# Kernel tuning notes

Measured on AMD Instinct MI355X. Metric: run time of the kernel, lower is better.

## Reference

```python
import jax, jax.numpy as jnp
import numpy as np

EMBED_DIM = 2048
NUM_HEADS = 16
NUM_HEADS_KV = 16
HEAD_DIM = EMBED_DIM // NUM_HEADS  # 128
ROT_DIM = HEAD_DIM // 2            # rotary_emb_dim = 64 (partial rotary)
ROPE_BASE = 10000.0
SEQLEN = 2048


def _rope_cos_sin(seqlen):
    # inv_freq over rotary dim (fp32 positions, as pos_idx_in_fp32=True)
    inv_freq = 1.0 / (ROPE_BASE ** (jnp.arange(0, ROT_DIM, 2, dtype=jnp.float32) / ROT_DIM))
    t = jnp.arange(seqlen, dtype=jnp.float32)
    freqs = jnp.outer(t, inv_freq)                 # (S, ROT_DIM//2)
    return jnp.cos(freqs), jnp.sin(freqs)


def _apply_rotary(x, cos, sin):
    # x: (B, S, H, D); non-interleaved (GPT-NeoX) rotary on first ROT_DIM dims
    rd = cos.shape[-1] * 2
    x_rot, x_pass = x[..., :rd], x[..., rd:]
    x1, x2 = x_rot[..., : rd // 2], x_rot[..., rd // 2 :]
    c = cos[None, :, None, :]
    s = sin[None, :, None, :]
    o1 = x1 * c - x2 * s
    o2 = x1 * s + x2 * c
    return jnp.concatenate([o1, o2, x_pass], axis=-1)


def setup_inputs() -> dict:
    key = jax.random.key(0)
    ks = jax.random.split(key, 5)
    scale_in = 1.0 / np.sqrt(EMBED_DIM)
    return {
        "x_q": jax.random.normal(ks[0], (SEQLEN, EMBED_DIM), dtype=jnp.float32),
        "Wqkv_w": jax.random.normal(ks[1], (HEAD_DIM * (NUM_HEADS + 2 * NUM_HEADS_KV), EMBED_DIM), dtype=jnp.float32) * scale_in,
        "Wqkv_b": jax.random.normal(ks[2], (HEAD_DIM * (NUM_HEADS + 2 * NUM_HEADS_KV),), dtype=jnp.float32) * 0.01,
        "Wo_w": jax.random.normal(ks[3], (EMBED_DIM, EMBED_DIM), dtype=jnp.float32) * scale_in,
        "Wo_b": jax.random.normal(ks[4], (EMBED_DIM,), dtype=jnp.float32) * 0.01,
    }


def reference(x_q, Wqkv_w, Wqkv_b, Wo_w, Wo_b):
    S = x_q.shape[0]
    H, Hkv, D = NUM_HEADS, NUM_HEADS_KV, HEAD_DIM
    # fused QKV projection
    qkv = x_q @ Wqkv_w.T + Wqkv_b                     # (S, (H+2Hkv)*D)
    q = qkv[:, : H * D].reshape(1, S, H, D)
    kv = qkv[:, H * D :].reshape(1, S, 2, Hkv, D)
    # rotary (q_position_ids = k_position_ids = arange(S))
    cos, sin = _rope_cos_sin(S)
    q = _apply_rotary(q, cos, sin)
    k = _apply_rotary(kv[:, :, 0], cos, sin)          # (1, S, Hkv, D)
    v = kv[:, :, 1]
    # causal attention, softmax scale 1/sqrt(D)
    scores = jnp.einsum("bshd,bthd->bhst", q, k) / jnp.sqrt(jnp.float32(D))
    causal = jnp.arange(S)[:, None] >= jnp.arange(S)[None, :]  # (S, S)
    scores = jnp.where(causal[None, None], scores, jnp.float32(-1e30))
    attn = jax.nn.softmax(scores, axis=-1)
    out = jnp.einsum("bhst,bthd->bshd", attn, v)      # (1, S, H, D)
    out = out.reshape(1, S, H * D)
    out = out @ Wo_w.T + Wo_b
    return out[0]                                     # (S, E)
```

## Files before the change

### kernel.cpp

```cpp
#include <hip/hip_runtime.h>
#include <stdint.h>

#define QKV_N 6144
#define ATT_SCALE 0.08838834764831845f

typedef __attribute__((ext_vector_type(8))) short short8;
typedef __attribute__((ext_vector_type(4))) float f32x4;

__device__ __forceinline__ uint16_t f2b(float x){
  uint32_t u = __float_as_uint(x);
  uint32_t r = (u + 0x7fffu + ((u >> 16) & 1u)) >> 16;
  return (uint16_t)r;
}
__device__ __forceinline__ float b2f(uint16_t h){
  return __uint_as_float(((uint32_t)h) << 16);
}
__device__ __forceinline__ void g2l16(const void* g, void* l){
  __builtin_amdgcn_global_load_lds((const __attribute__((address_space(1))) void*)g,
                                   (__attribute__((address_space(3))) void*)l, 16, 0, 0);
}

__device__ __forceinline__ void cvt8(const float* __restrict__ in, uint16_t* __restrict__ out, int i){
  const float4* p = (const float4*)in;
  float4 a = p[2*i], b = p[2*i+1];
  union { short8 v; uint16_t u[8]; } o;
  o.u[0]=f2b(a.x); o.u[1]=f2b(a.y); o.u[2]=f2b(a.z); o.u[3]=f2b(a.w);
  o.u[4]=f2b(b.x); o.u[5]=f2b(b.y); o.u[6]=f2b(b.z); o.u[7]=f2b(b.w);
  ((short8*)out)[i] = o.v;
}

__global__ __launch_bounds__(256) void k_prep(const float* __restrict__ x,
                                              const float* __restrict__ wqkv,
                                              const float* __restrict__ wo,
                                              uint16_t* __restrict__ xb,
                                              uint16_t* __restrict__ wqkvb,
                                              uint16_t* __restrict__ wob,
                                              float* __restrict__ ct,
                                              float* __restrict__ st){
  const int b = blockIdx.x, tid = threadIdx.x;
  if (b < 2048) {
    cvt8(x, xb, b*256 + tid);
  } else if (b < 8192) {
    cvt8(wqkv, wqkvb, (b - 2048)*256 + tid);
  } else if (b < 10240) {
    cvt8(wo, wob, (b - 8192)*256 + tid);
  } else {
    int i = (b - 10240)*256 + tid;
    int s = i >> 5, d = i & 31;
    float inv = __expf(-(float)d * (9.210340371976184f / 32.0f));
    float f = (float)s * inv;
    ct[i] = cosf(f);
    st[i] = sinf(f);
  }
}

__global__ __launch_bounds__(512, 1) void k_gemmA(const uint16_t* __restrict__ A,
                                                  const uint16_t* __restrict__ B,
                                                  const float* __restrict__ bias,
                                                  uint16_t* __restrict__ C){
  __shared__ uint16_t As[3*4096];
  __shared__ uint16_t Bs[3*6144];
  const int K = 2048, N = 6144;

  const int wg = blockIdx.x;
  const int xcd = wg & 7, bi = wg >> 3;
  const int m0 = (xcd*2 + (bi & 1)) * 128;
  const int n0 = (bi >> 1) * 192;

  const int tid = threadIdx.x;
  const int wid = tid >> 6, l = tid & 63;
  const int wm = wid >> 2, wn = wid & 3;
  const int g = l >> 4, c = l & 15;

  const int rpA = tid >> 3, sA = (tid & 7) ^ (rpA & 7);
  const size_t srcA0 = (size_t)(m0 + rpA*2 + (sA >> 2)) * K + (sA & 3) * 8;
  const size_t srcB0 = (size_t)(n0 + rpA*2 + (sA >> 2)) * K + (sA & 3) * 8;
  const int rpB2 = 64 + (tid >> 3), sB2 = (tid & 7) ^ (rpB2 & 7);
  const size_t srcB1 = (size_t)(n0 + rpB2*2 + (sB2 >> 2)) * K + (sB2 & 3) * 8;

  const int pg   = ((c & 1) << 2) | g;
  const int slb  = (pg ^ ((c >> 1) & 7)) << 3;
  const int rpa0 = wm*32 + (c >> 1);
  const int rpb0 = wn*24 + (c >> 1);

  f32x4 acc[4][3] = {};
  const int NT = K >> 5;

  #pragma unroll
  for (int t0 = 0; t0 < 2; ++t0) {
    g2l16(A + srcA0 + t0*32, (void*)(As + t0*4096 + tid*8));
    g2l16(B + srcB0 + t0*32, (void*)(Bs + t0*6144 + tid*8));
    if (tid < 256)
      g2l16(B + srcB1 + t0*32, (void*)(Bs + t0*6144 + 4096 + tid*8));
  }
  if (wid < 4) { asm volatile("s_waitcnt vmcnt(3)" ::: "memory"); }
  else         { asm volatile("s_waitcnt vmcnt(2)" ::: "memory"); }
  __builtin_amdgcn_s_barrier();

  #pragma unroll 3
  for (int t = 0; t < NT; ++t) {
    const uint16_t* __restrict__ Ab = As + (t % 3)*4096;
    const uint16_t* __restrict__ Bb = Bs + (t % 3)*6144;
    const int t2 = t + 2;

    short8 av[4], bv[3];
    #pragma unroll
    for (int mi = 0; mi < 4; ++mi)
      av[mi] = *(const short8*)&Ab[(rpa0 + mi*8)*64 + slb];
    #pragma unroll
    for (int ni = 0; ni < 3; ++ni)
      bv[ni] = *(const short8*)&Bb[(rpb0 + ni*8)*64 + slb];
    if (t2 < NT) {
      const int b2 = (t2 % 3);
      g2l16(A + srcA0 + t2*32, (void*)(As + b2*4096 + tid*8));
      g2l16(B + srcB0 + t2*32, (void*)(Bs + b2*6144 + tid*8));
      if (tid < 256)
        g2l16(B + srcB1 + t2*32, (void*)(Bs + b2*6144 + 4096 + tid*8));
    }
    __builtin_amdgcn_s_barrier();
    __builtin_amdgcn_s_setprio(1);
    #pragma unroll
    for (int mi = 0; mi < 4; ++mi)
      #pragma unroll
      for (int ni = 0; ni < 3; ++ni)
        acc[mi][ni] = __builtin_amdgcn_mfma_f32_16x16x32_bf16(av[mi], bv[ni], acc[mi][ni], 0, 0, 0);
    __builtin_amdgcn_s_setprio(0);
    if (wid < 4) { asm volatile("s_waitcnt vmcnt(3)" ::: "memory"); }
    else         { asm volatile("s_waitcnt vmcnt(2)" ::: "memory"); }
    __builtin_amdgcn_s_barrier();
  }

  #pragma unroll
  for (int ni = 0; ni < 3; ++ni) {
    const int col = n0 + wn*48 + ni*16 + c;
    const float bvl = bias[col];
    #pragma unroll
    for (int mi = 0; mi < 4; ++mi) {
      const int row0 = m0 + wm*64 + mi*16 + g*4;
      #pragma unroll
      for (int j = 0; j < 4; ++j)
        C[(size_t)(row0 + j)*N + col] = f2b(acc[mi][ni][j] + bvl);
    }
  }
}

__global__ __launch_bounds__(256, 2) void k_gemm128(const uint16_t* __restrict__ A,
                                                    const uint16_t* __restrict__ B,
                                                    const float* __restrict__ bias,
                                                    float* __restrict__ C,
                                                    int M, int N, int K){
  __shared__ uint16_t As[3*4096];
  __shared__ uint16_t Bs[3*2048];

  const int wg = blockIdx.x;
  const int xcd = wg & 7, bi = wg >> 3;
  const int m0 = (xcd*2 + (bi & 1)) * 128;
  const int n0 = (bi >> 1) * 64;

  const int tid = threadIdx.x;
  const int wid = tid >> 6, l = tid & 63;
  const int wm = wid >> 1, wn = wid & 1;
  const int g = l >> 4, c = l & 15;

  const int rpA1 = tid >> 3, sA1 = (tid & 7) ^ (rpA1 & 7);
  const size_t srcA0 = (size_t)(m0 + rpA1*2 + (sA1 >> 2)) * K + (sA1 & 3) * 8;
  const int rpA2 = 32 + (tid >> 3), sA2 = (tid & 7) ^ (rpA2 & 7);
  const size_t srcA1 = (size_t)(m0 + rpA2*2 + (sA2 >> 2)) * K + (sA2 & 3) * 8;
  const int rpB = tid >> 3, sB = (tid & 7) ^ (rpB & 7);
  const size_t srcB0 = (size_t)(n0 + rpB*2 + (sB >> 2)) * K + (sB & 3) * 8;

  const int pg  = ((c & 1) << 2) | g;
  const int slb = (pg ^ ((c >> 1) & 7)) << 3;
  const int ra0 = wm*32 + (c >> 1);
  const int rb0 = wn*16 + (c >> 1);

  f32x4 acc[4][2] = {};
  const int NT = K >> 5;

  #pragma unroll
  for (int t0 = 0; t0 < 2; ++t0) {
    g2l16(A + srcA0 + t0*32, (void*)(As + t0*4096 + tid*8));
    g2l16(A + srcA1 + t0*32, (void*)(As + t0*4096 + 2048 + tid*8));
    g2l16(B + srcB0 + t0*32, (void*)(Bs + t0*2048 + tid*8));
  }
  asm volatile("s_waitcnt vmcnt(3)" ::: "memory");
  __builtin_amdgcn_s_barrier();

  #pragma unroll 3
  for (int t = 0; t < NT; ++t) {
    const uint16_t* __restrict__ Ab = As + (t % 3)*4096;
    const uint16_t* __restrict__ Bb = Bs + (t % 3)*2048;
    const int t2 = t + 2;

    short8 av[4], bv[2];
    #pragma unroll
    for (int mi = 0; mi < 4; ++mi)
      av[mi] = *(const short8*)&Ab[(ra0 + mi*8)*64 + slb];
    #pragma unroll
    for (int ni = 0; ni < 2; ++ni)
      bv[ni] = *(const short8*)&Bb[(rb0 + ni*8)*64 + slb];
    if (t2 < NT) {
      const int b2 = (t2 % 3);
      g2l16(A + srcA0 + t2*32, (void*)(As + b2*4096 + tid*8));
      g2l16(A + srcA1 + t2*32, (void*)(As + b2*4096 + 2048 + tid*8));
      g2l16(B + srcB0 + t2*32, (void*)(Bs + b2*2048 + tid*8));
    }
    __builtin_amdgcn_s_barrier();
    __builtin_amdgcn_s_setprio(1);
    #pragma unroll
    for (int mi = 0; mi < 4; ++mi)
      #pragma unroll
      for (int ni = 0; ni < 2; ++ni)
        acc[mi][ni] = __builtin_amdgcn_mfma_f32_16x16x32_bf16(av[mi], bv[ni], acc[mi][ni], 0, 0, 0);
    __builtin_amdgcn_s_setprio(0);
    asm volatile("s_waitcnt vmcnt(3)" ::: "memory");
    __builtin_amdgcn_s_barrier();
  }

  #pragma unroll
  for (int ni = 0; ni < 2; ++ni) {
    const int col = n0 + wn*32 + ni*16 + c;
    const float bvl = bias[col];
    #pragma unroll
    for (int mi = 0; mi < 4; ++mi) {
      const int row0 = m0 + wm*64 + mi*16 + g*4;
      #pragma unroll
      for (int j = 0; j < 4; ++j)
        C[(size_t)(row0 + j)*N + col] = acc[mi][ni][j] + bvl;
    }
  }
}

__global__ __launch_bounds__(256) void k_rope_vt(const uint16_t* __restrict__ qkv,
                                                 const float* __restrict__ ct,
                                                 const float* __restrict__ st,
                                                 uint16_t* __restrict__ qo,
                                                 uint16_t* __restrict__ ko,
                                                 uint16_t* __restrict__ vt){
  const int blk = blockIdx.x, tid = threadIdx.x;
  if (blk < 4096) {
    int idx = blk * 256 + tid;
    int db = idx & 15;
    int s  = (idx >> 4) & 2047;
    int h  = (idx >> 15) & 15;
    int which = idx >> 19;
    const uint16_t* src = qkv + (size_t)s * QKV_N + which * 2048 + h * 128;
    uint16_t* dst = (which ? ko : qo) + (((size_t)(h*2048 + s)) << 7) + db*8;
    const float scale = which ? 1.0f : ATT_SCALE;
    int d0 = db * 8;
    union { short8 v; uint16_t u[8]; } o;
    if (d0 >= 64) {
      short8 xv = *(const short8*)(src + d0);
      #pragma unroll
      for (int e = 0; e < 8; ++e) o.u[e] = f2b(b2f((uint16_t)xv[e]) * scale);
    } else {
      int dd = d0 & 31;
      short8 a = *(const short8*)(src + dd);
      short8 b = *(const short8*)(src + dd + 32);
      float4 c0 = *(const float4*)(ct + s*32 + dd);
      float4 c1 = *(const float4*)(ct + s*32 + dd + 4);
      float4 s0 = *(const float4*)(st + s*32 + dd);
      float4 s1 = *(const float4*)(st + s*32 + dd + 4);
      float cc[8] = {c0.x,c0.y,c0.z,c0.w,c1.x,c1.y,c1.z,c1.w};
      float ss[8] = {s0.x,s0.y,s0.z,s0.w,s1.x,s1.y,s1.z,s1.w};
      #pragma unroll
      for (int e = 0; e < 8; ++e) {
        float x1 = b2f((uint16_t)a[e]), x2 = b2f((uint16_t)b[e]);
        float v = (d0 < 32) ? (x1*cc[e] - x2*ss[e]) : (x1*ss[e] + x2*cc[e]);
        o.u[e] = f2b(v * scale);
      }
    }
    *(short8*)dst = o.v;
  } else {
    __shared__ uint16_t tl[64][80];
    const int b = blk - 4096;
    const int st_ = b & 31, dt = (b >> 5) & 1, h = b >> 6;
    const int s_l = tid >> 2, cch = (tid & 3) * 16;
    const uint16_t* src = qkv + (size_t)(st_*64 + s_l) * QKV_N + 4096 + h*128 + dt*64 + cch;
    short8 a = *(const short8*)src;
    short8 b2 = *(const short8*)(src + 8);
    #pragma unroll
    for (int e = 0; e < 8; ++e) {
      tl[cch + e][s_l]     = (uint16_t)a[e];
      tl[cch + 8 + e][s_l] = (uint16_t)b2[e];
    }
    __syncthreads();
    const int d_l = tid >> 2;
    uint16_t* dst = vt + ((size_t)h << 18) + (size_t)(dt*64 + d_l) * 2048 + st_*64 + cch;
    *(short8*)dst       = *(const short8*)&tl[d_l][cch];
    *(short8*)(dst + 8) = *(const short8*)&tl[d_l][cch + 8];
  }
}

__global__ __launch_bounds__(512, 1) void k_attn(const uint16_t* __restrict__ Q,
                                                 const uint16_t* __restrict__ Kb,
                                                 const uint16_t* __restrict__ Vtg,
                                                 uint16_t* __restrict__ Out){
  __shared__ uint16_t Ks[2][2][64*128];
  __shared__ uint16_t Vs[2][2][128*64];
  __shared__ uint16_t Ps[8][16*88];

  const int bid = blockIdx.x;
  const int lin = (bid & 7) * 32 + (bid >> 3);
  const int h = lin >> 4;
  const int pair = lin & 15;

  const int tid = threadIdx.x, w = tid >> 6, l = tid & 63;
  const int gid = w >> 2, wq = w & 3;
  const int tg = tid & 255;
  const int g = l >> 4, c = l & 15;
  const int swz = (c & 7) << 4;

  const uint16_t* __restrict__ Qh = Q   + ((size_t)h << 18);
  const uint16_t* __restrict__ Kh = Kb  + ((size_t)h << 18);
  const uint16_t* __restrict__ Vh = Vtg + ((size_t)h << 18);
  float* scratch = (float*)&Ks[0][0][0];

  int koff[4], voff[4];
  #pragma unroll
  for (int j = 0; j < 4; ++j) {
    int kr = j*16 + (tg >> 4);
    koff[j] = kr*128 + (((tg & 15) ^ (kr & 7)) << 3);
    int vd = j*32 + (tg >> 3);
    voff[j] = vd*2048 + (((tg & 7) ^ (vd & 7)) << 3);
  }

  uint16_t* KsG = &Ks[gid][0][0];
  uint16_t* VsG = &Vs[gid][0][0];

  #pragma unroll 1
  for (int half = 0; half < 2; ++half) {
    const int qt = half ? (31 - pair) : pair;
    const int nt = qt + 1;
    const int nsteps = (nt + 1) >> 1;
    const int qrow = qt*64 + wq*16 + c;

    short8 qf[4];
    #pragma unroll
    for (int t = 0; t < 4; ++t)
      qf[t] = *(const short8*)&Qh[(size_t)qrow*128 + t*32 + g*8];

    f32x4 acc[8] = {};
    float mrow[4], lrow[4];
    #pragma unroll
    for (int j = 0; j < 4; ++j) { mrow[j] = -3e38f; lrow[j] = 0.0f; }

    if (gid < nt) {
      #pragma unroll
      for (int j = 0; j < 4; ++j) {
        g2l16(Kh + (size_t)gid*8192 + koff[j], (void*)(KsG + j*2048 + tg*8));
        g2l16(Vh + gid*64 + voff[j],           (void*)(VsG + j*2048 + tg*8));
      }
    }
    asm volatile("s_waitcnt vmcnt(0)" ::: "memory");
    __syncthreads();

    #pragma unroll 1
    for (int step = 0; step < nsteps; ++step) {
      const int kt = 2*step + gid;
      const int cur = step & 1;
      if (kt + 2 < nt) {
        const int k1 = kt + 2;
        #pragma unroll
        for (int j = 0; j < 4; ++j) {
          g2l16(Kh + (size_t)k1*8192 + koff[j], (void*)(KsG + (cur^1)*8192 + j*2048 + tg*8));
          g2l16(Vh + k1*64 + voff[j],           (void*)(VsG + (cur^1)*8192 + j*2048 + tg*8));
        }
      }

      if (kt < nt) {
        const int k0 = kt * 64;
        const uint16_t* Kcur = KsG + cur*8192;
        const uint16_t* Vcur = VsG + cur*8192;

        f32x4 sc4[4] = {};
        #pragma unroll
        for (int ct2 = 0; ct2 < 4; ++ct2) {
          const char* krp = (const char*)Kcur + (ct2*16 + c)*256;
          #pragma unroll
          for (int t = 0; t < 4; ++t) {
            short8 kb = *(const short8*)(krp + ((t*64 + g*16) ^ swz));
            sc4[ct2] = __builtin_amdgcn_mfma_f32_16x16x32_bf16(qf[t], kb, sc4[ct2], 0, 0, 0);
          }
        }

        const bool lastt = (kt == nt - 1);
        #pragma unroll
        for (int j = 0; j < 4; ++j) {
          const int qg = qt*64 + wq*16 + g*4 + j;
          float v0 = sc4[0][j], v1 = sc4[1][j], v2 = sc4[2][j], v3 = sc4[3][j];
          if (lastt) {
            if (k0 +      c > qg) v0 = -3e38f;
            if (k0 + 16 + c > qg) v1 = -3e38f;
            if (k0 + 32 + c > qg) v2 = -3e38f;
            if (k0 + 48 + c > qg) v3 = -3e38f;
          }
          float t0 = fmaxf(fmaxf(v0, v1), fmaxf(v2, v3));
          #pragma unroll
          for (int d2 = 1; d2 < 16; d2 <<= 1) t0 = fmaxf(t0, __shfl_xor(t0, d2, 64));
          const float mn = fmaxf(mrow[j], t0);
          const float scl = __expf(mrow[j] - mn);
          const float p0 = __expf(v0 - mn), p1 = __expf(v1 - mn),
                      p2 = __expf(v2 - mn), p3 = __expf(v3 - mn);
          float rs = (p0 + p1) + (p2 + p3);
          #pragma unroll
          for (int d2 = 1; d2 < 16; d2 <<= 1) rs += __shfl_xor(rs, d2, 64);
          lrow[j] = lrow[j]*scl + rs;
          mrow[j] = mn;
          #pragma unroll
          for (int n = 0; n < 8; ++n) acc[n][j] *= scl;
          uint16_t* pw = &Ps[w][(g*4 + j)*88];
          pw[c] = f2b(p0); pw[16+c] = f2b(p1); pw[32+c] = f2b(p2); pw[48+c] = f2b(p3);
        }

        #pragma unroll
        for (int kk = 0; kk < 2; ++kk) {
          short8 pf = *(const short8*)&Ps[w][c*88 + kk*32 + g*8];
          #pragma unroll
          for (int n = 0; n < 8; ++n) {
            const char* vrp = (const char*)Vcur + (n*16 + c)*128;
            short8 vf = *(const short8*)(vrp + ((kk*64 + g*16) ^ swz));
            acc[n] = __builtin_amdgcn_mfma_f32_16x16x32_bf16(pf, vf, acc[n], 0, 0, 0);
          }
        }
      }

      asm volatile("s_waitcnt vmcnt(0)" ::: "memory");
      __syncthreads();
    }

    float* Up = scratch + wq * 2112;
    if (gid == 1) {
      #pragma unroll
      for (int j = 0; j < 4; ++j) {
        const int row = g*4 + j;
        #pragma unroll
        for (int n = 0; n < 8; ++n)
          Up[row*128 + n*16 + c] = acc[n][j];
        if (c == 0) { Up[2048 + row] = mrow[j]; Up[2064 + row] = lrow[j]; }
      }
    }
    __syncthreads();
    if (gid == 0) {
      #pragma unroll
      for (int j = 0; j < 4; ++j) {
        const int row = g*4 + j;
        const int qg = qt*64 + wq*16 + row;
        const float mB = Up[2048 + row], lB = Up[2064 + row];
        const float mn = fmaxf(mrow[j], mB);
        const float e1 = __expf(mrow[j] - mn);
        const float e2 = __expf(mB - mn);
        const float inv = 1.0f / (lrow[j]*e1 + lB*e2);
        #pragma unroll
        for (int n = 0; n < 8; ++n) {
          const float u = acc[n][j]*e1 + Up[row*128 + n*16 + c]*e2;
          Out[(size_t)qg*2048 + h*128 + n*16 + c] = f2b(u * inv);
        }
      }
    }
    __syncthreads();
  }
}

extern "C" void kernel_launch(void* const* d_in, const int* in_sizes, int n_in,
                              void* d_out, int out_size, void* d_ws, size_t ws_size,
                              hipStream_t stream){
  const float* x    = (const float*)d_in[0];
  const float* Wqkv = (const float*)d_in[1];
  const float* bqkv = (const float*)d_in[2];
  const float* Wo   = (const float*)d_in[3];
  const float* bo   = (const float*)d_in[4];

  char* ws = (char*)d_ws;
  uint16_t* q_bf    = (uint16_t*)(ws);
  uint16_t* k_bf    = (uint16_t*)(ws + 8388608);
  uint16_t* vt_bf   = (uint16_t*)(ws + 16777216);
  uint16_t* attn_bf = (uint16_t*)(ws + 25165824);
  uint16_t* x_bf    = attn_bf;
  uint16_t* wqkv_bf = (uint16_t*)(ws + 33554432);
  uint16_t* wo_bf   = (uint16_t*)(ws + 58720256);
  uint16_t* qkv_bf  = (uint16_t*)(ws + 67108864);
  float*    cos_t   = (float*)(ws + 92274688);
  float*    sin_t   = (float*)(ws + 92536832);

  k_prep<<<dim3(10496), dim3(256), 0, stream>>>(x, Wqkv, Wo, x_bf, wqkv_bf, wo_bf,
                                                cos_t, sin_t);
  k_gemmA<<<dim3(512), dim3(512), 0, stream>>>(x_bf, wqkv_bf, bqkv, qkv_bf);
  k_rope_vt<<<dim3(5120), dim3(256), 0, stream>>>(qkv_bf, cos_t, sin_t, q_bf, k_bf, vt_bf);
  k_attn<<<dim3(256), dim3(512), 0, stream>>>(q_bf, k_bf, vt_bf, attn_bf);
  k_gemm128<<<dim3(512), dim3(256), 0, stream>>>(attn_bf, wo_bf, bo, (float*)d_out,
                                                 2048, 2048, 2048);
}
```

Measured before the change: 175.8 us.

## Enlarge output GEMM tile with 4-stage pipeline; lazy softmax rescale in attention

The output projection GEMM moves from 256-thread 128x64 tiles with a 3-stage buffer to 512-thread 128x128 tiles with a 4-stage buffer. This halves the grid and raises operand reuse per block. The attention kernel skips the cross-lane max reduction and accumulator rescale whenever every row's new local max stays within 8 of the running max, and defers the row-sum shuffle reduction to the end. It also raises wave priority around the MFMA sections. The lazy rescale lets exponentials grow up to e^8 before renormalising, and fewer, larger GEMM blocks may leave some CUs idle.

```diff
diff --git a/kernel.cpp b/kernel.cpp
--- a/kernel.cpp
+++ b/kernel.cpp
@@ -144,30 +144,27 @@
   }
 }
 
-__global__ __launch_bounds__(256, 2) void k_gemm128(const uint16_t* __restrict__ A,
+__global__ __launch_bounds__(512, 1) void k_gemm128(const uint16_t* __restrict__ A,
                                                     const uint16_t* __restrict__ B,
                                                     const float* __restrict__ bias,
                                                     float* __restrict__ C,
                                                     int M, int N, int K){
-  __shared__ uint16_t As[3*4096];
-  __shared__ uint16_t Bs[3*2048];
+  __shared__ uint16_t As[4*4096];
+  __shared__ uint16_t Bs[4*4096];
 
   const int wg = blockIdx.x;
   const int xcd = wg & 7, bi = wg >> 3;
   const int m0 = (xcd*2 + (bi & 1)) * 128;
-  const int n0 = (bi >> 1) * 64;
+  const int n0 = (bi >> 1) * 128;
 
   const int tid = threadIdx.x;
   const int wid = tid >> 6, l = tid & 63;
-  const int wm = wid >> 1, wn = wid & 1;
+  const int wm = wid >> 2, wn = wid & 3;
   const int g = l >> 4, c = l & 15;
 
-  const int rpA1 = tid >> 3, sA1 = (tid & 7) ^ (rpA1 & 7);
-  const size_t srcA0 = (size_t)(m0 + rpA1*2 + (sA1 >> 2)) * K + (sA1 & 3) * 8;
-  const int rpA2 = 32 + (tid >> 3), sA2 = (tid & 7) ^ (rpA2 & 7);
-  const size_t srcA1 = (size_t)(m0 + rpA2*2 + (sA2 >> 2)) * K + (sA2 & 3) * 8;
-  const int rpB = tid >> 3, sB = (tid & 7) ^ (rpB & 7);
-  const size_t srcB0 = (size_t)(n0 + rpB*2 + (sB >> 2)) * K + (sB & 3) * 8;
+  const int rp_s = tid >> 3, q_s = tid & 7, s_s = q_s ^ (rp_s & 7);
+  const int srcA = (m0 + rp_s*2 + (s_s >> 2)) * K + (s_s & 3) * 8;
+  const int srcB = (n0 + rp_s*2 + (s_s >> 2)) * K + (s_s & 3) * 8;
 
   const int pg  = ((c & 1) << 2) | g;
   const int slb = (pg ^ ((c >> 1) & 7)) << 3;
@@ -178,19 +175,19 @@
   const int NT = K >> 5;
 
   #pragma unroll
-  for (int t0 = 0; t0 < 2; ++t0) {
-    g2l16(A + srcA0 + t0*32, (void*)(As + t0*4096 + tid*8));
-    g2l16(A + srcA1 + t0*32, (void*)(As + t0*4096 + 2048 + tid*8));
-    g2l16(B + srcB0 + t0*32, (void*)(Bs + t0*2048 + tid*8));
-  }
-  asm volatile("s_waitcnt vmcnt(3)" ::: "memory");
+  for (int t0 = 0; t0 < 3; ++t0) {
+    g2l16(A + srcA + t0*32, (void*)(As + t0*4096 + tid*8));
+    g2l16(B + srcB + t0*32, (void*)(Bs + t0*4096 + tid*8));
+  }
+  asm volatile("s_waitcnt vmcnt(4)" ::: "memory");
   __builtin_amdgcn_s_barrier();
 
-  #pragma unroll 3
+  #pragma unroll 4
   for (int t = 0; t < NT; ++t) {
-    const uint16_t* __restrict__ Ab = As + (t % 3)*4096;
-    const uint16_t* __restrict__ Bb = Bs + (t % 3)*2048;
-    const int t2 = t + 2;
+    const uint16_t* __restrict__ Ab = As + (t & 3)*4096;
+    const uint16_t* __restrict__ Bb = Bs + (t & 3)*4096;
+    const int t3 = t + 3;
+    const int b3 = (t3 & 3)*4096;
 
     short8 av[4], bv[2];
     #pragma unroll
@@ -199,11 +196,9 @@
     #pragma unroll
     for (int ni = 0; ni < 2; ++ni)
       bv[ni] = *(const short8*)&Bb[(rb0 + ni*8)*64 + slb];
-    if (t2 < NT) {
-      const int b2 = (t2 % 3);
-      g2l16(A + srcA0 + t2*32, (void*)(As + b2*4096 + tid*8));
-      g2l16(A + srcA1 + t2*32, (void*)(As + b2*4096 + 2048 + tid*8));
-      g2l16(B + srcB0 + t2*32, (void*)(Bs + b2*2048 + tid*8));
+    if (t3 < NT) {
+      g2l16(A + srcA + t3*32, (void*)(As + b3 + tid*8));
+      g2l16(B + srcB + t3*32, (void*)(Bs + b3 + tid*8));
     }
     __builtin_amdgcn_s_barrier();
     __builtin_amdgcn_s_setprio(1);
@@ -213,7 +208,7 @@
       for (int ni = 0; ni < 2; ++ni)
         acc[mi][ni] = __builtin_amdgcn_mfma_f32_16x16x32_bf16(av[mi], bv[ni], acc[mi][ni], 0, 0, 0);
     __builtin_amdgcn_s_setprio(0);
-    asm volatile("s_waitcnt vmcnt(3)" ::: "memory");
+    asm volatile("s_waitcnt vmcnt(4)" ::: "memory");
     __builtin_amdgcn_s_barrier();
   }
 
@@ -341,9 +336,9 @@
       qf[t] = *(const short8*)&Qh[(size_t)qrow*128 + t*32 + g*8];
 
     f32x4 acc[8] = {};
-    float mrow[4], lrow[4];
-    #pragma unroll
-    for (int j = 0; j < 4; ++j) { mrow[j] = -3e38f; lrow[j] = 0.0f; }
+    float mrow[4], lsum[4];
+    #pragma unroll
+    for (int j = 0; j < 4; ++j) { mrow[j] = -3e38f; lsum[j] = 0.0f; }
 
     if (gid < nt) {
       #pragma unroll
@@ -374,6 +369,7 @@
         const uint16_t* Vcur = VsG + cur*8192;
 
         f32x4 sc4[4] = {};
+        __builtin_amdgcn_s_setprio(1);
         #pragma unroll
         for (int ct2 = 0; ct2 < 4; ++ct2) {
           const char* krp = (const char*)Kcur + (ct2*16 + c)*256;
@@ -383,8 +379,12 @@
             sc4[ct2] = __builtin_amdgcn_mfma_f32_16x16x32_bf16(qf[t], kb, sc4[ct2], 0, 0, 0);
           }
         }
+        __builtin_amdgcn_s_setprio(0);
 
         const bool lastt = (kt == nt - 1);
+        float va[4][4];
+        float m4[4];
+        int fastok = 1;
         #pragma unroll
         for (int j = 0; j < 4; ++j) {
           const int qg = qt*64 + wq*16 + g*4 + j;
@@ -395,24 +395,41 @@
             if (k0 + 32 + c > qg) v2 = -3e38f;
             if (k0 + 48 + c > qg) v3 = -3e38f;
           }
-          float t0 = fmaxf(fmaxf(v0, v1), fmaxf(v2, v3));
+          va[j][0] = v0; va[j][1] = v1; va[j][2] = v2; va[j][3] = v3;
+          float m = fmaxf(fmaxf(fmaxf(v0, v1), v2), v3);
+          m4[j] = m;
+          fastok &= (m <= mrow[j] + 8.0f) ? 1 : 0;
+        }
+        if (__all(fastok)) {
           #pragma unroll
-          for (int d2 = 1; d2 < 16; d2 <<= 1) t0 = fmaxf(t0, __shfl_xor(t0, d2, 64));
-          const float mn = fmaxf(mrow[j], t0);
-          const float scl = __expf(mrow[j] - mn);
-          const float p0 = __expf(v0 - mn), p1 = __expf(v1 - mn),
-                      p2 = __expf(v2 - mn), p3 = __expf(v3 - mn);
-          float rs = (p0 + p1) + (p2 + p3);
+          for (int j = 0; j < 4; ++j) {
+            const float mj = mrow[j];
+            const float p0 = __expf(va[j][0] - mj), p1 = __expf(va[j][1] - mj),
+                        p2 = __expf(va[j][2] - mj), p3 = __expf(va[j][3] - mj);
+            lsum[j] += (p0 + p1) + (p2 + p3);
+            uint16_t* pw = &Ps[w][(g*4 + j)*88];
+            pw[c] = f2b(p0); pw[16+c] = f2b(p1); pw[32+c] = f2b(p2); pw[48+c] = f2b(p3);
+          }
+        } else {
           #pragma unroll
-          for (int d2 = 1; d2 < 16; d2 <<= 1) rs += __shfl_xor(rs, d2, 64);
-          lrow[j] = lrow[j]*scl + rs;
-          mrow[j] = mn;
-          #pragma unroll
-          for (int n = 0; n < 8; ++n) acc[n][j] *= scl;
-          uint16_t* pw = &Ps[w][(g*4 + j)*88];
-          pw[c] = f2b(p0); pw[16+c] = f2b(p1); pw[32+c] = f2b(p2); pw[48+c] = f2b(p3);
+          for (int j = 0; j < 4; ++j) {
+            float t0 = m4[j];
+            #pragma unroll
+            for (int d2 = 1; d2 < 16; d2 <<= 1) t0 = fmaxf(t0, __shfl_xor(t0, d2, 64));
+            const float mn = fmaxf(mrow[j], t0);
+            const float scl = __expf(mrow[j] - mn);
+            const float p0 = __expf(va[j][0] - mn), p1 = __expf(va[j][1] - mn),
+                        p2 = __expf(va[j][2] - mn), p3 = __expf(va[j][3] - mn);
+            lsum[j] = lsum[j]*scl + (p0 + p1) + (p2 + p3);
+            mrow[j] = mn;
+            #pragma unroll
+            for (int n = 0; n < 8; ++n) acc[n][j] *= scl;
+            uint16_t* pw = &Ps[w][(g*4 + j)*88];
+            pw[c] = f2b(p0); pw[16+c] = f2b(p1); pw[32+c] = f2b(p2); pw[48+c] = f2b(p3);
+          }
         }
 
+        __builtin_amdgcn_s_setprio(1);
         #pragma unroll
         for (int kk = 0; kk < 2; ++kk) {
           short8 pf = *(const short8*)&Ps[w][c*88 + kk*32 + g*8];
@@ -423,10 +440,20 @@
             acc[n] = __builtin_amdgcn_mfma_f32_16x16x32_bf16(pf, vf, acc[n], 0, 0, 0);
           }
         }
+        __builtin_amdgcn_s_setprio(0);
       }
 
       asm volatile("s_waitcnt vmcnt(0)" ::: "memory");
       __syncthreads();
+    }
+
+    float lrow[4];
+    #pragma unroll
+    for (int j = 0; j < 4; ++j) {
+      float rs = lsum[j];
+      #pragma unroll
+      for (int d2 = 1; d2 < 16; d2 <<= 1) rs += __shfl_xor(rs, d2, 64);
+      lrow[j] = rs;
     }
 
     float* Up = scratch + wq * 2112;
@@ -488,6 +515,6 @@
   k_gemmA<<<dim3(512), dim3(512), 0, stream>>>(x_bf, wqkv_bf, bqkv, qkv_bf);
   k_rope_vt<<<dim3(5120), dim3(256), 0, stream>>>(qkv_bf, cos_t, sin_t, q_bf, k_bf, vt_bf);
   k_attn<<<dim3(256), dim3(512), 0, stream>>>(q_bf, k_bf, vt_bf, attn_bf);
-  k_gemm128<<<dim3(512), dim3(256), 0, stream>>>(attn_bf, wo_bf, bo, (float*)d_out,
+  k_gemm128<<<dim3(256), dim3(512), 0, stream>>>(attn_bf, wo_bf, bo, (float*)d_out,
                                                  2048, 2048, 2048);
 }
```

New measurement: 165.2 us (median of 3 runs). 6.1% less time.
